# Kernel optimization log

Measured on AMD Instinct MI355X. Metric: run time of the kernel, lower is better.

## Reference

```python
import jax, jax.numpy as jnp
import numpy as np


def _graph_conv_mean(x, src, dst, edge_weight, W_rel, W_root, b, num_nodes):
    # messages: gather source features, optionally scale by edge weight
    msg = x[src]  # [E, D]
    if edge_weight is not None:
        msg = msg * edge_weight[:, None]
    # mean aggregation over incoming edges per destination node
    summed = jax.ops.segment_sum(msg, dst, num_segments=num_nodes)  # [N, D]
    count = jax.ops.segment_sum(jnp.ones((src.shape[0],), x.dtype), dst, num_segments=num_nodes)
    mean = summed / jnp.maximum(count, 1.0)[:, None]
    # out = lin_rel(mean) + lin_root(x) + bias
    return mean @ W_rel + x @ W_root + b


def setup_inputs() -> dict:
    key = jax.random.key(0)
    ks = jax.random.split(key, 8)
    N, E, D, H, C = 100000, 1600000, 128, 32, 5
    x = jax.random.normal(ks[0], (N, D), dtype=jnp.float32)
    edge_index = jax.random.randint(ks[1], (2, E), 0, N, dtype=jnp.int64)
    edge_weight = jax.random.uniform(ks[2], (E,), dtype=jnp.float32)
    W_rel1 = jax.random.normal(ks[3], (D, H), dtype=jnp.float32) / np.sqrt(D)
    W_root1 = jax.random.normal(ks[4], (D, H), dtype=jnp.float32) / np.sqrt(D)
    b1 = jnp.zeros((H,), jnp.float32)
    W_rel2 = jax.random.normal(ks[5], (H, C), dtype=jnp.float32) / np.sqrt(H)
    W_root2 = jax.random.normal(ks[6], (H, C), dtype=jnp.float32) / np.sqrt(H)
    b2 = jnp.zeros((C,), jnp.float32)
    return {"x": x, "edge_index": edge_index, "edge_weight": edge_weight,
            "W_rel1": W_rel1, "W_root1": W_root1, "b1": b1,
            "W_rel2": W_rel2, "W_root2": W_root2, "b2": b2}


def reference(x, edge_index, edge_weight, W_rel1, W_root1, b1, W_rel2, W_root2, b2):
    N = x.shape[0]
    src, dst = edge_index[0], edge_index[1]
    # conv1 with edge_weight
    h = _graph_conv_mean(x, src, dst, edge_weight, W_rel1, W_root1, b1, N)
    h = jax.nn.relu(h)
    # dropout is identity at inference (training=False)
    # conv2 without edge_weight
    out = _graph_conv_mean(h, src, dst, None, W_rel2, W_root2, b2, N)
    return jax.nn.log_softmax(out, axis=1)
```

## Files before the change

kernel.cpp:

```cpp
#include <hip/hip_runtime.h>
#include <math.h>

#define N_NODES 100000
#define E_EDGES 1600000
#define D_IN    128
#define H_MID   32
#define C_OUT   5

#define BSHIFT 9
#define BNODES 512
#define NBKT   196
#define BCAP   9200
#define SRC_BITS 17
#define SRC_MASK 0x1FFFF

#define KP 136

typedef __attribute__((ext_vector_type(8))) short bf16x8;
typedef __attribute__((ext_vector_type(4))) float f32x4;

__device__ inline unsigned f2bf(float f) {
    unsigned u = __float_as_uint(f);
    return (u + 0x7FFFu + ((u >> 16) & 1u)) >> 16;
}

__global__ void k_prep(const float* __restrict__ Wrel,
                       const float* __restrict__ Wroot,
                       int* __restrict__ bucket_cursor,
                       unsigned short* __restrict__ wt_g) {
    int tid = threadIdx.x;
    bucket_cursor[tid] = 0;
    for (int i = tid; i < 64 * 128; i += 256) {
        int n = i >> 7, k = i & 127;
        float v = (n < H_MID) ? Wrel[k * H_MID + n] : Wroot[k * H_MID + (n - H_MID)];
        wt_g[i] = (unsigned short)f2bf(v);
    }
}

__global__ __launch_bounds__(256) void k1_mfma(
    const float* __restrict__ x,
    const unsigned short* __restrict__ wt_g,
    const float* __restrict__ b1,
    unsigned short* __restrict__ xrelh,
    float* __restrict__ xroot) {
    __shared__ unsigned short xs[64 * KP];
    int tid = threadIdx.x;
    int nodeBase = blockIdx.x * 64;

    #pragma unroll
    for (int it = 0; it < 16; ++it) {
        int idx = it * 256 + tid;
        int row = idx >> 6, kp = idx & 63;
        int node = nodeBase + row;
        float2 v = make_float2(0.f, 0.f);
        if (node < N_NODES)
            v = *(const float2*)(x + (size_t)node * D_IN + kp * 2);
        unsigned pk = f2bf(v.x) | (f2bf(v.y) << 16);
        *(unsigned*)(xs + row * KP + kp * 2) = pk;
    }
    __syncthreads();

    int lane = tid & 63;
    int wv = tid >> 6;
    int m = lane & 15;
    int quad = lane >> 4;

    f32x4 acc[4];
    #pragma unroll
    for (int nt = 0; nt < 4; ++nt) acc[nt] = (f32x4){0.f, 0.f, 0.f, 0.f};

    #pragma unroll
    for (int kk = 0; kk < 4; ++kk) {
        int k0 = kk * 32 + quad * 8;
        bf16x8 a = *(const bf16x8*)(xs + (wv * 16 + m) * KP + k0);
        #pragma unroll
        for (int nt = 0; nt < 4; ++nt) {
            bf16x8 b = *(const bf16x8*)(wt_g + (nt * 16 + m) * 128 + k0);
            acc[nt] = __builtin_amdgcn_mfma_f32_16x16x32_bf16(a, b, acc[nt], 0, 0, 0);
        }
    }

    #pragma unroll
    for (int nt = 0; nt < 4; ++nt) {
        #pragma unroll
        for (int r = 0; r < 4; ++r) {
            int node = nodeBase + wv * 16 + quad * 4 + r;
            int colg = nt * 16 + m;
            if (node < N_NODES) {
                if (colg < H_MID) {
                    xrelh[(size_t)node * H_MID + colg] =
                        (unsigned short)f2bf(acc[nt][r]);
                } else {
                    int c = colg - H_MID;
                    xroot[(size_t)node * H_MID + c] = acc[nt][r] + b1[c];
                }
            }
        }
    }
}

__global__ __launch_bounds__(1024) void k_binA(
    const int* __restrict__ src,
    const int* __restrict__ dst,
    const float* __restrict__ ew,
    int* __restrict__ bucket_cursor,
    int2* __restrict__ staged) {
    __shared__ int cnt[NBKT];
    __shared__ int lstart[NBKT];
    __shared__ int gbase[NBKT];
    __shared__ int scanbuf[256];
    __shared__ int2 ebuf[2048];
    __shared__ short bbuf[2048];
    int tid = threadIdx.x;
    int eBase = blockIdx.x * 2048;

    if (tid < NBKT) cnt[tid] = 0;
    __syncthreads();

    int b[2], rank[2], packed[2], wbits[2];
    bool valid[2];
    #pragma unroll
    for (int u = 0; u < 2; ++u) {
        int e = eBase + u * 1024 + tid;
        valid[u] = (e < E_EDGES);
        b[u] = 0; rank[u] = 0; packed[u] = 0; wbits[u] = 0;
        if (valid[u]) {
            int d = dst[e];
            int s = src[e];
            wbits[u] = __float_as_int(ew[e]);
            b[u] = d >> BSHIFT;
            packed[u] = ((d & (BNODES - 1)) << SRC_BITS) | s;
            rank[u] = atomicAdd(&cnt[b[u]], 1);
        }
    }
    __syncthreads();

    if (tid < 256) scanbuf[tid] = (tid < NBKT) ? cnt[tid] : 0;
    __syncthreads();
    for (int off = 1; off < 256; off <<= 1) {
        int t = 0;
        if (tid < 256 && tid >= off) t = scanbuf[tid - off];
        __syncthreads();
        if (tid < 256) scanbuf[tid] += t;
        __syncthreads();
    }
    if (tid < NBKT) {
        lstart[tid] = scanbuf[tid] - cnt[tid];
        gbase[tid]  = atomicAdd(&bucket_cursor[tid], cnt[tid]);
    }
    __syncthreads();
    int total = scanbuf[NBKT - 1];

    #pragma unroll
    for (int u = 0; u < 2; ++u) {
        if (valid[u]) {
            int slot = lstart[b[u]] + rank[u];
            ebuf[slot] = make_int2(packed[u], wbits[u]);
            bbuf[slot] = (short)b[u];
        }
    }
    __syncthreads();

    for (int t = tid; t < total; t += 1024) {
        int2 ev = ebuf[t];
        int bb = bbuf[t];
        int gpos = gbase[bb] + (t - lstart[bb]);
        if (gpos < BCAP)
            staged[(size_t)bb * BCAP + gpos] = ev;
    }
}

__global__ __launch_bounds__(1024) void k_binB2(
    const int* __restrict__ bucket_cursor,
    const int2* __restrict__ staged,
    int* __restrict__ deg,
    int* __restrict__ offsets,
    int2* __restrict__ csr8) {
    __shared__ int hist[BNODES];
    __shared__ int scanb[BNODES];
    __shared__ int cur[BNODES];
    __shared__ int sbase[256];
    int tid = threadIdx.x;
    int b = blockIdx.x;

    if (tid < 256) {
        int c = (tid < NBKT) ? bucket_cursor[tid] : 0;
        sbase[tid] = (c > BCAP) ? BCAP : c;
    }
    if (tid < BNODES) hist[tid] = 0;
    __syncthreads();
    for (int off = 1; off < 256; off <<= 1) {
        int t = 0;
        if (tid < 256 && tid >= off) t = sbase[tid - off];
        __syncthreads();
        if (tid < 256) sbase[tid] += t;
        __syncthreads();
    }
    int count = bucket_cursor[b];
    if (count > BCAP) count = BCAP;
    int base = sbase[b] - count;
    int nodeBase = b << BSHIFT;
    const int2* sp = staged + (size_t)b * BCAP;

    for (int i = tid; i < count; i += 1024)
        atomicAdd(&hist[((unsigned)sp[i].x) >> SRC_BITS], 1);
    __syncthreads();

    int v = 0;
    if (tid < BNODES) {
        v = hist[tid];
        scanb[tid] = v;
    }
    __syncthreads();
    for (int off = 1; off < BNODES; off <<= 1) {
        int t = 0;
        if (tid < BNODES && tid >= off) t = scanb[tid - off];
        __syncthreads();
        if (tid < BNODES) scanb[tid] += t;
        __syncthreads();
    }
    if (tid < BNODES) {
        int excl = scanb[tid] - v;
        int node = nodeBase + tid;
        if (node < N_NODES) {
            deg[node]     = v;
            offsets[node] = base + excl;
        }
        cur[tid] = excl;
    }
    __syncthreads();

    for (int i = tid; i < count; i += 1024) {
        int2 ev = sp[i];
        int local = ((unsigned)ev.x) >> SRC_BITS;
        int pos = atomicAdd(&cur[local], 1);
        csr8[base + pos] = make_int2(ev.x & SRC_MASK, ev.y);
    }
}

__global__ __launch_bounds__(512) void k_layer1(
    const int* __restrict__ offsets,
    const int* __restrict__ deg,
    const int2* __restrict__ csr8,
    const unsigned short* __restrict__ xrelh,
    const float* __restrict__ xroot,
    const float* __restrict__ Wrel2,
    const float* __restrict__ Wroot2,
    const float* __restrict__ b2,
    float* __restrict__ h2rel,
    float* __restrict__ h2root) {
    int node = blockIdx.x * 32 + (threadIdx.x >> 4);
    int lane = threadIdx.x & 15;
    int beg = offsets[node];
    int dg  = deg[node];
    int end = beg + dg;

    float acc0 = 0.f, acc1 = 0.f;
    int i = beg;
    for (; i + 8 <= end; i += 8) {
        int2 e[8];
        unsigned v[8];
        #pragma unroll
        for (int u = 0; u < 8; ++u) e[u] = csr8[i + u];
        #pragma unroll
        for (int u = 0; u < 8; ++u)
            v[u] = *(const unsigned*)(xrelh + (size_t)e[u].x * H_MID + lane * 2);
        #pragma unroll
        for (int u = 0; u < 8; ++u) {
            float w = __int_as_float(e[u].y);
            acc0 += __uint_as_float((v[u] & 0xFFFFu) << 16) * w;
            acc1 += __uint_as_float(v[u] & 0xFFFF0000u) * w;
        }
    }
    for (; i < end; ++i) {
        int2 e0 = csr8[i];
        unsigned v0 = *(const unsigned*)(xrelh + (size_t)e0.x * H_MID + lane * 2);
        float w0 = __int_as_float(e0.y);
        acc0 += __uint_as_float((v0 & 0xFFFFu) << 16) * w0;
        acc1 += __uint_as_float(v0 & 0xFFFF0000u) * w0;
    }

    float inv = 1.0f / fmaxf((float)dg, 1.0f);
    float2 rt = *(const float2*)(xroot + (size_t)node * H_MID + lane * 2);
    float h0 = fmaxf(acc0 * inv + rt.x, 0.f);
    float h1 = fmaxf(acc1 * inv + rt.y, 0.f);

    float p[2 * C_OUT];
    #pragma unroll
    for (int j = 0; j < C_OUT; ++j) {
        p[j]         = h0 * Wrel2[(2 * lane) * C_OUT + j]
                     + h1 * Wrel2[(2 * lane + 1) * C_OUT + j];
        p[C_OUT + j] = h0 * Wroot2[(2 * lane) * C_OUT + j]
                     + h1 * Wroot2[(2 * lane + 1) * C_OUT + j];
    }
    #pragma unroll
    for (int mm = 8; mm > 0; mm >>= 1) {
        #pragma unroll
        for (int j = 0; j < 2 * C_OUT; ++j)
            p[j] += __shfl_xor(p[j], mm, 16);
    }
    if (lane == 0) {
        #pragma unroll
        for (int j = 0; j < C_OUT; ++j) {
            h2rel[(size_t)node * C_OUT + j]  = p[j];
            h2root[(size_t)node * C_OUT + j] = p[C_OUT + j] + b2[j];
        }
    }
}

__global__ __launch_bounds__(256) void k_layer2(
    const int* __restrict__ offsets,
    const int* __restrict__ deg,
    const int2* __restrict__ csr8,
    const float* __restrict__ h2rel,
    const float* __restrict__ h2root,
    float* __restrict__ out) {
    int node = blockIdx.x * 32 + (threadIdx.x >> 3);
    int lane = threadIdx.x & 7;
    int beg = offsets[node];
    int dg  = deg[node];
    int end = beg + dg;

    float acc = 0.f;
    if (lane < C_OUT) {
        int i = beg;
        for (; i + 8 <= end; i += 8) {
            int s[8];
            float v[8];
            #pragma unroll
            for (int u = 0; u < 8; ++u) s[u] = csr8[i + u].x;
            #pragma unroll
            for (int u = 0; u < 8; ++u)
                v[u] = h2rel[(size_t)s[u] * C_OUT + lane];
            #pragma unroll
            for (int u = 0; u < 8; ++u) acc += v[u];
        }
        for (; i < end; ++i)
            acc += h2rel[(size_t)csr8[i].x * C_OUT + lane];
    }
    float inv = 1.0f / fmaxf((float)dg, 1.0f);
    float o = (lane < C_OUT)
                  ? acc * inv + h2root[(size_t)node * C_OUT + lane]
                  : -INFINITY;
    float m = o;
    #pragma unroll
    for (int dd = 4; dd > 0; dd >>= 1) m = fmaxf(m, __shfl_xor(m, dd, 8));
    float e = (lane < C_OUT) ? expf(o - m) : 0.f;
    float ssum = e;
    #pragma unroll
    for (int dd = 4; dd > 0; dd >>= 1) ssum += __shfl_xor(ssum, dd, 8);
    float lse = m + logf(ssum);
    if (lane < C_OUT)
        out[(size_t)node * C_OUT + lane] = o - lse;
}

extern "C" void kernel_launch(void* const* d_in, const int* in_sizes, int n_in,
                              void* d_out, int out_size, void* d_ws, size_t ws_size,
                              hipStream_t stream) {
    const float* x      = (const float*)d_in[0];
    const int*   ei     = (const int*)d_in[1];
    const float* ew     = (const float*)d_in[2];
    const float* Wrel1  = (const float*)d_in[3];
    const float* Wroot1 = (const float*)d_in[4];
    const float* b1     = (const float*)d_in[5];
    const float* Wrel2  = (const float*)d_in[6];
    const float* Wroot2 = (const float*)d_in[7];
    const float* b2     = (const float*)d_in[8];
    float* out = (float*)d_out;

    const int* src = ei;
    const int* dst = ei + E_EDGES;

    char* ws = (char*)d_ws;
    int*   deg           = (int*)ws;
    int*   bucket_cursor = deg + N_NODES;
    unsigned short* wt_g = (unsigned short*)(bucket_cursor + 256);
    int*   offsets       = (int*)(wt_g + 64 * 128);
    int2*  csr8          = (int2*)(offsets + N_NODES);
    unsigned short* xrelh = (unsigned short*)(csr8 + E_EDGES);
    float* xroot         = (float*)(xrelh + (size_t)N_NODES * H_MID);
    float* h2rel         = xroot + (size_t)N_NODES * H_MID;
    float* h2root        = h2rel + (size_t)N_NODES * C_OUT;
    int2*  staged        = (int2*)xrelh;

    k_prep<<<1, 256, 0, stream>>>(Wrel1, Wroot1, bucket_cursor, wt_g);

    k_binA<<<(E_EDGES + 2047) / 2048, 1024, 0, stream>>>(src, dst, ew,
                                                         bucket_cursor, staged);
    k_binB2<<<NBKT, 1024, 0, stream>>>(bucket_cursor, staged,
                                       deg, offsets, csr8);

    k1_mfma<<<(N_NODES + 63) / 64, 256, 0, stream>>>(x, wt_g, b1,
                                                     xrelh, xroot);

    k_layer1<<<N_NODES / 32, 512, 0, stream>>>(offsets, deg, csr8,
                                               xrelh, xroot, Wrel2, Wroot2, b2,
                                               h2rel, h2root);

    k_layer2<<<N_NODES / 32, 256, 0, stream>>>(offsets, deg, csr8,
                                               h2rel, h2root, out);
}
```

Measured before the change: 222.5 us.

## Split CSR into SoA src/fp16 weight arrays and store root term in bf16

Edge weights are stored as fp16 in a separate array, and the staged and CSR buffers change from interleaved int2 to separate int source and ushort weight arrays. Layer 2 then reads only 4 bytes per edge instead of 8, and layer 1 reads 6. The root projection xroot is stored as bf16 instead of fp32, halving that traffic. The cost is lower precision for edge weights and the root term, plus extra separate store and load streams in the binning kernels.

After: 226.3 us. No clear change (+1.7%).

```diff
diff --git a/kernel.cpp b/kernel.cpp
--- a/kernel.cpp
+++ b/kernel.cpp
@@ -1,4 +1,5 @@
 #include <hip/hip_runtime.h>
+#include <hip/hip_fp16.h>
 #include <math.h>
 
 #define N_NODES 100000
@@ -22,6 +23,15 @@
 __device__ inline unsigned f2bf(float f) {
     unsigned u = __float_as_uint(f);
     return (u + 0x7FFFu + ((u >> 16) & 1u)) >> 16;
+}
+__device__ inline float bf2f(unsigned v) { return __uint_as_float(v << 16); }
+__device__ inline unsigned short f2h(float f) {
+    __half h = __float2half(f);
+    return *(unsigned short*)&h;
+}
+__device__ inline float h2f(unsigned short u) {
+    __half h = *(__half*)&u;
+    return __half2float(h);
 }
 
 __global__ void k_prep(const float* __restrict__ Wrel,
@@ -42,7 +52,7 @@
     const unsigned short* __restrict__ wt_g,
     const float* __restrict__ b1,
     unsigned short* __restrict__ xrelh,
-    float* __restrict__ xroot) {
+    unsigned short* __restrict__ xrooth) {
     __shared__ unsigned short xs[64 * KP];
     int tid = threadIdx.x;
     int nodeBase = blockIdx.x * 64;
@@ -92,7 +102,8 @@
                         (unsigned short)f2bf(acc[nt][r]);
                 } else {
                     int c = colg - H_MID;
-                    xroot[(size_t)node * H_MID + c] = acc[nt][r] + b1[c];
+                    xrooth[(size_t)node * H_MID + c] =
+                        (unsigned short)f2bf(acc[nt][r] + b1[c]);
                 }
             }
         }
@@ -104,12 +115,14 @@
     const int* __restrict__ dst,
     const float* __restrict__ ew,
     int* __restrict__ bucket_cursor,
-    int2* __restrict__ staged) {
+    int* __restrict__ staged_p,
+    unsigned short* __restrict__ staged_w) {
     __shared__ int cnt[NBKT];
     __shared__ int lstart[NBKT];
     __shared__ int gbase[NBKT];
     __shared__ int scanbuf[256];
-    __shared__ int2 ebuf[2048];
+    __shared__ int ebuf_p[2048];
+    __shared__ unsigned short ebuf_w[2048];
     __shared__ short bbuf[2048];
     int tid = threadIdx.x;
     int eBase = blockIdx.x * 2048;
@@ -117,17 +130,18 @@
     if (tid < NBKT) cnt[tid] = 0;
     __syncthreads();
 
-    int b[2], rank[2], packed[2], wbits[2];
+    int b[2], rank[2], packed[2];
+    unsigned short wh[2];
     bool valid[2];
     #pragma unroll
     for (int u = 0; u < 2; ++u) {
         int e = eBase + u * 1024 + tid;
         valid[u] = (e < E_EDGES);
-        b[u] = 0; rank[u] = 0; packed[u] = 0; wbits[u] = 0;
+        b[u] = 0; rank[u] = 0; packed[u] = 0; wh[u] = 0;
         if (valid[u]) {
             int d = dst[e];
             int s = src[e];
-            wbits[u] = __float_as_int(ew[e]);
+            wh[u] = f2h(ew[e]);
             b[u] = d >> BSHIFT;
             packed[u] = ((d & (BNODES - 1)) << SRC_BITS) | s;
             rank[u] = atomicAdd(&cnt[b[u]], 1);
@@ -155,27 +169,32 @@
     for (int u = 0; u < 2; ++u) {
         if (valid[u]) {
             int slot = lstart[b[u]] + rank[u];
-            ebuf[slot] = make_int2(packed[u], wbits[u]);
+            ebuf_p[slot] = packed[u];
+            ebuf_w[slot] = wh[u];
             bbuf[slot] = (short)b[u];
         }
     }
     __syncthreads();
 
     for (int t = tid; t < total; t += 1024) {
-        int2 ev = ebuf[t];
         int bb = bbuf[t];
         int gpos = gbase[bb] + (t - lstart[bb]);
-        if (gpos < BCAP)
-            staged[(size_t)bb * BCAP + gpos] = ev;
+        if (gpos < BCAP) {
+            size_t idx = (size_t)bb * BCAP + gpos;
+            staged_p[idx] = ebuf_p[t];
+            staged_w[idx] = ebuf_w[t];
+        }
     }
 }
 
 __global__ __launch_bounds__(1024) void k_binB2(
     const int* __restrict__ bucket_cursor,
-    const int2* __restrict__ staged,
+    const int* __restrict__ staged_p,
+    const unsigned short* __restrict__ staged_w,
     int* __restrict__ deg,
     int* __restrict__ offsets,
-    int2* __restrict__ csr8) {
+    int* __restrict__ csr_src,
+    unsigned short* __restrict__ csr_w) {
     __shared__ int hist[BNODES];
     __shared__ int scanb[BNODES];
     __shared__ int cur[BNODES];
@@ -200,10 +219,11 @@
     if (count > BCAP) count = BCAP;
     int base = sbase[b] - count;
     int nodeBase = b << BSHIFT;
-    const int2* sp = staged + (size_t)b * BCAP;
+    const int* sp = staged_p + (size_t)b * BCAP;
+    const unsigned short* sw = staged_w + (size_t)b * BCAP;
 
     for (int i = tid; i < count; i += 1024)
-        atomicAdd(&hist[((unsigned)sp[i].x) >> SRC_BITS], 1);
+        atomicAdd(&hist[((unsigned)sp[i]) >> SRC_BITS], 1);
     __syncthreads();
 
     int v = 0;
@@ -231,19 +251,22 @@
     __syncthreads();
 
     for (int i = tid; i < count; i += 1024) {
-        int2 ev = sp[i];
-        int local = ((unsigned)ev.x) >> SRC_BITS;
+        int p = sp[i];
+        unsigned short w = sw[i];
+        int local = ((unsigned)p) >> SRC_BITS;
         int pos = atomicAdd(&cur[local], 1);
-        csr8[base + pos] = make_int2(ev.x & SRC_MASK, ev.y);
+        csr_src[base + pos] = p & SRC_MASK;
+        csr_w[base + pos]   = w;
     }
 }
 
 __global__ __launch_bounds__(512) void k_layer1(
     const int* __restrict__ offsets,
     const int* __restrict__ deg,
-    const int2* __restrict__ csr8,
+    const int* __restrict__ csr_src,
+    const unsigned short* __restrict__ csr_w,
     const unsigned short* __restrict__ xrelh,
-    const float* __restrict__ xroot,
+    const unsigned short* __restrict__ xrooth,
     const float* __restrict__ Wrel2,
     const float* __restrict__ Wroot2,
     const float* __restrict__ b2,
@@ -258,32 +281,35 @@
     float acc0 = 0.f, acc1 = 0.f;
     int i = beg;
     for (; i + 8 <= end; i += 8) {
-        int2 e[8];
+        int s[8];
+        unsigned short wh[8];
         unsigned v[8];
         #pragma unroll
-        for (int u = 0; u < 8; ++u) e[u] = csr8[i + u];
+        for (int u = 0; u < 8; ++u) s[u] = csr_src[i + u];
+        #pragma unroll
+        for (int u = 0; u < 8; ++u) wh[u] = csr_w[i + u];
         #pragma unroll
         for (int u = 0; u < 8; ++u)
-            v[u] = *(const unsigned*)(xrelh + (size_t)e[u].x * H_MID + lane * 2);
+            v[u] = *(const unsigned*)(xrelh + (size_t)s[u] * H_MID + lane * 2);
         #pragma unroll
         for (int u = 0; u < 8; ++u) {
-            float w = __int_as_float(e[u].y);
-            acc0 += __uint_as_float((v[u] & 0xFFFFu) << 16) * w;
+            float w = h2f(wh[u]);
+            acc0 += bf2f(v[u] & 0xFFFFu) * w;
             acc1 += __uint_as_float(v[u] & 0xFFFF0000u) * w;
         }
     }
     for (; i < end; ++i) {
-        int2 e0 = csr8[i];
-        unsigned v0 = *(const unsigned*)(xrelh + (size_t)e0.x * H_MID + lane * 2);
-        float w0 = __int_as_float(e0.y);
-        acc0 += __uint_as_float((v0 & 0xFFFFu) << 16) * w0;
+        int s0 = csr_src[i];
+        float w0 = h2f(csr_w[i]);
+        unsigned v0 = *(const unsigned*)(xrelh + (size_t)s0 * H_MID + lane * 2);
+        acc0 += bf2f(v0 & 0xFFFFu) * w0;
         acc1 += __uint_as_float(v0 & 0xFFFF0000u) * w0;
     }
 
     float inv = 1.0f / fmaxf((float)dg, 1.0f);
-    float2 rt = *(const float2*)(xroot + (size_t)node * H_MID + lane * 2);
-    float h0 = fmaxf(acc0 * inv + rt.x, 0.f);
-    float h1 = fmaxf(acc1 * inv + rt.y, 0.f);
+    unsigned rtv = *(const unsigned*)(xrooth + (size_t)node * H_MID + lane * 2);
+    float h0 = fmaxf(acc0 * inv + bf2f(rtv & 0xFFFFu), 0.f);
+    float h1 = fmaxf(acc1 * inv + __uint_as_float(rtv & 0xFFFF0000u), 0.f);
 
     float p[2 * C_OUT];
     #pragma unroll
@@ -311,7 +337,7 @@
 __global__ __launch_bounds__(256) void k_layer2(
     const int* __restrict__ offsets,
     const int* __restrict__ deg,
-    const int2* __restrict__ csr8,
+    const int* __restrict__ csr_src,
     const float* __restrict__ h2rel,
     const float* __restrict__ h2root,
     float* __restrict__ out) {
@@ -328,7 +354,7 @@
             int s[8];
             float v[8];
             #pragma unroll
-            for (int u = 0; u < 8; ++u) s[u] = csr8[i + u].x;
+            for (int u = 0; u < 8; ++u) s[u] = csr_src[i + u];
             #pragma unroll
             for (int u = 0; u < 8; ++u)
                 v[u] = h2rel[(size_t)s[u] * C_OUT + lane];
@@ -336,7 +362,7 @@
             for (int u = 0; u < 8; ++u) acc += v[u];
         }
         for (; i < end; ++i)
-            acc += h2rel[(size_t)csr8[i].x * C_OUT + lane];
+            acc += h2rel[(size_t)csr_src[i] * C_OUT + lane];
     }
     float inv = 1.0f / fmaxf((float)dg, 1.0f);
     float o = (lane < C_OUT)
@@ -376,27 +402,30 @@
     int*   bucket_cursor = deg + N_NODES;
     unsigned short* wt_g = (unsigned short*)(bucket_cursor + 256);
     int*   offsets       = (int*)(wt_g + 64 * 128);
-    int2*  csr8          = (int2*)(offsets + N_NODES);
-    unsigned short* xrelh = (unsigned short*)(csr8 + E_EDGES);
-    float* xroot         = (float*)(xrelh + (size_t)N_NODES * H_MID);
-    float* h2rel         = xroot + (size_t)N_NODES * H_MID;
+    int*   csr_src       = offsets + N_NODES;
+    unsigned short* csr_w = (unsigned short*)(csr_src + E_EDGES);
+    unsigned short* xrelh = csr_w + E_EDGES;
+    unsigned short* xrooth = xrelh + (size_t)N_NODES * H_MID;
+    float* h2rel         = (float*)(xrooth + (size_t)N_NODES * H_MID);
     float* h2root        = h2rel + (size_t)N_NODES * C_OUT;
-    int2*  staged        = (int2*)xrelh;
+    int*   staged_p      = (int*)xrelh;
+    unsigned short* staged_w = (unsigned short*)(staged_p + (size_t)NBKT * BCAP);
 
     k_prep<<<1, 256, 0, stream>>>(Wrel1, Wroot1, bucket_cursor, wt_g);
 
     k_binA<<<(E_EDGES + 2047) / 2048, 1024, 0, stream>>>(src, dst, ew,
-                                                         bucket_cursor, staged);
-    k_binB2<<<NBKT, 1024, 0, stream>>>(bucket_cursor, staged,
-                                       deg, offsets, csr8);
+                                                         bucket_cursor,
+                                                         staged_p, staged_w);
+    k_binB2<<<NBKT, 1024, 0, stream>>>(bucket_cursor, staged_p, staged_w,
+                                       deg, offsets, csr_src, csr_w);
 
     k1_mfma<<<(N_NODES + 63) / 64, 256, 0, stream>>>(x, wt_g, b1,
-                                                     xrelh, xroot);
-
-    k_layer1<<<N_NODES / 32, 512, 0, stream>>>(offsets, deg, csr8,
-                                               xrelh, xroot, Wrel2, Wroot2, b2,
+                                                     xrelh, xrooth);
+
+    k_layer1<<<N_NODES / 32, 512, 0, stream>>>(offsets, deg, csr_src, csr_w,
+                                               xrelh, xrooth, Wrel2, Wroot2, b2,
                                                h2rel, h2root);
 
-    k_layer2<<<N_NODES / 32, 256, 0, stream>>>(offsets, deg, csr8,
+    k_layer2<<<N_NODES / 32, 256, 0, stream>>>(offsets, deg, csr_src,
                                                h2rel, h2root, out);
 }
```
